# Optimization experiments

Measured on AMD Instinct MI355X. Metric: run time of the kernel, lower is better.

Reference implementation:

```python
import jax, jax.numpy as jnp
import numpy as np

B = 4            # batch size (max batch index + 1, fixed by construction)
H, W = 176, 200  # feature_map_size; x in [0,H), y in [0,W)
C_IN, C_OUT = 128, 256
BW, N = 4096, 64
EPS = 1e-5       # torch LayerNorm default


def setup_inputs() -> dict:
    key = jax.random.key(0)
    k1, k2, k3, k4, k5, k6, k7 = jax.random.split(key, 7)
    window_features = jax.random.normal(k1, (BW, N, C_IN), jnp.float32)
    bidx = jax.random.randint(k2, (BW, N, 1), 0, B)
    xidx = jax.random.randint(k3, (BW, N, 1), -8, H + 8)   # includes invalid coords
    yidx = jax.random.randint(k4, (BW, N, 1), -8, W + 8)
    window_indices = jnp.concatenate([bidx, xidx, yidx], axis=-1).astype(jnp.int32)
    norm_weight = 1.0 + 0.1 * jax.random.normal(k5, (C_IN,), jnp.float32)
    norm_bias = 0.1 * jax.random.normal(k6, (C_IN,), jnp.float32)
    lin_weight = jax.random.normal(k7, (C_OUT, C_IN), jnp.float32) / np.sqrt(C_IN)
    return {"window_features": window_features, "window_indices": window_indices,
            "norm_weight": norm_weight, "norm_bias": norm_bias, "lin_weight": lin_weight}


def reference(window_features, window_indices, norm_weight, norm_bias, lin_weight):
    # window_features: (BW, N, C_IN); window_indices: (BW, N, 3) = (batch, x, y)
    bw, n, c = window_features.shape
    feats = window_features.reshape(-1, c)                # (P, C)
    idx = window_indices.reshape(-1, 3)
    b, x, y = idx[:, 0], idx[:, 1], idx[:, 2]
    valid = (x >= 0) & (x < H) & (y >= 0) & (y < W)

    # unique + index_add_ + sparse-to-dense == scatter-add into dense BEV grid.
    # Invalid rows are routed out-of-bounds and dropped.
    bs = jnp.where(valid, b, B)
    xs = jnp.where(valid, x, 0)
    ys = jnp.where(valid, y, 0)
    # dense layout matches spconv: spatial_shape=[W, H], indices (b, y, x)
    dense_sum = jnp.zeros((B, W, H, c), window_features.dtype)
    dense_sum = dense_sum.at[bs, ys, xs].add(feats, mode="drop")
    count = jnp.zeros((B, W, H), window_features.dtype)
    count = count.at[bs, ys, xs].add(1.0, mode="drop")
    occupied = count > 0                                   # cells holding a unique voxel

    # LayerNorm over C (patch_norm=True) then Linear (bias=False) on occupied cells
    mu = jnp.mean(dense_sum, axis=-1, keepdims=True)
    var = jnp.mean(jnp.square(dense_sum - mu), axis=-1, keepdims=True)
    normed = (dense_sum - mu) * jax.lax.rsqrt(var + EPS) * norm_weight + norm_bias
    dense_out = jnp.einsum("bwhc,oc->bwho", normed, lin_weight)
    dense_out = jnp.where(occupied[..., None], dense_out, 0.0)  # empty cells stay zero

    # gather_operation: pull dense features back to each valid window point
    gathered = dense_out[jnp.where(valid, b, 0), ys, xs]   # (P, C_OUT)
    new_feats = jnp.where(valid[:, None], gathered, 0.0).reshape(bw, n, C_OUT)
    return new_feats, window_indices
```

## Files before the change

kernel.cpp:

```cpp
#include <hip/hip_runtime.h>
#include <stdint.h>

#define HH 176
#define WW 200
#define BB 4
#define CIN 128
#define COUT 256
#define NPTS (4096 * 64)
#define CELLS (BB * WW * HH)
#define FEAT_OUT_ELEMS ((size_t)NPTS * COUT)
#define CAP 32

typedef __attribute__((ext_vector_type(8))) short bf16x8;
typedef __attribute__((ext_vector_type(4))) float f32x4;

__device__ __forceinline__ unsigned short f2bf(float f) {
    union { float f; unsigned int u; } c; c.f = f;
    unsigned int u = c.u;
    u += 0x7fffu + ((u >> 16) & 1u);
    return (unsigned short)(u >> 16);
}
__device__ __forceinline__ float bf2f(unsigned int h16) {
    union { unsigned int u; float f; } c; c.u = h16 << 16;
    return c.f;
}

__global__ __launch_bounds__(256) void build_kernel(
    const int* __restrict__ idx, int* __restrict__ counts, int* __restrict__ plist)
{
    int p = blockIdx.x * 256 + threadIdx.x;
    int b = idx[3 * p], x = idx[3 * p + 1], y = idx[3 * p + 2];
    if ((unsigned)x < HH && (unsigned)y < WW) {
        int cell = (b * WW + y) * HH + x;
        int slot = atomicAdd(&counts[cell], 1);
        if (slot < CAP) plist[(size_t)cell * CAP + slot] = p;
    }
}

__global__ __launch_bounds__(256) void cell_kernel(
    const float* __restrict__ feats, const int* __restrict__ counts,
    const int* __restrict__ plist,
    const float* __restrict__ nw, const float* __restrict__ nb,
    unsigned short* __restrict__ normed)
{
    int cell = blockIdx.x * 4 + (threadIdx.x >> 6);
    int lane = threadIdx.x & 63;
    int n = counts[cell]; n = n < CAP ? n : CAP;
    const int* pl = plist + (size_t)cell * CAP;
    float a0 = 0.0f, a1 = 0.0f;
    for (int i = 0; i < n; ++i) {
        int pid = pl[i];
        float2 v = *(const float2*)(feats + (size_t)pid * CIN + lane * 2);
        a0 += v.x; a1 += v.y;
    }
    float s = a0 + a1;
    float ss = a0 * a0 + a1 * a1;
    #pragma unroll
    for (int m = 32; m >= 1; m >>= 1) {
        s  += __shfl_xor(s, m, 64);
        ss += __shfl_xor(ss, m, 64);
    }
    float mu  = s * (1.0f / 128.0f);
    float var = ss * (1.0f / 128.0f) - mu * mu;
    float inv = rsqrtf(var + 1e-5f);
    float w0 = nw[lane * 2], w1 = nw[lane * 2 + 1];
    float b0 = nb[lane * 2], b1 = nb[lane * 2 + 1];
    ushort2 st;
    st.x = f2bf((a0 - mu) * inv * w0 + b0);
    st.y = f2bf((a1 - mu) * inv * w1 + b1);
    *(ushort2*)(normed + (size_t)cell * CIN + lane * 2) = st;
}

__global__ __launch_bounds__(256) void wcvt_kernel(
    const float* __restrict__ lw, unsigned short* __restrict__ wb)
{
    int i = blockIdx.x * 256 + threadIdx.x;
    wb[i] = f2bf(lw[i]);
}

__global__ __launch_bounds__(256) void gemm_kernel(
    const unsigned short* __restrict__ A,
    const unsigned short* __restrict__ Wb,
    unsigned short* __restrict__ C)
{
    int n0 = blockIdx.x * 64;
    int w = threadIdx.x >> 6;
    int lane = threadIdx.x & 63;
    int l15 = lane & 15;
    int kgrp = (lane >> 4) * 8;

    f32x4 acc[4][4];
    #pragma unroll
    for (int i = 0; i < 4; ++i)
        #pragma unroll
        for (int j = 0; j < 4; ++j)
            acc[i][j] = (f32x4){0.0f, 0.0f, 0.0f, 0.0f};

    const unsigned short* arow[4];
    const unsigned short* brow[4];
    #pragma unroll
    for (int i = 0; i < 4; ++i)
        arow[i] = Wb + (size_t)(((w * 4 + i) * 16 + l15) * CIN) + kgrp;
    #pragma unroll
    for (int j = 0; j < 4; ++j)
        brow[j] = A + (size_t)(n0 + j * 16 + l15) * CIN + kgrp;

    #pragma unroll
    for (int kk = 0; kk < 4; ++kk) {
        bf16x8 a[4], b[4];
        #pragma unroll
        for (int i = 0; i < 4; ++i) a[i] = *(const bf16x8*)(arow[i] + kk * 32);
        #pragma unroll
        for (int j = 0; j < 4; ++j) b[j] = *(const bf16x8*)(brow[j] + kk * 32);
        #pragma unroll
        for (int i = 0; i < 4; ++i)
            #pragma unroll
            for (int j = 0; j < 4; ++j)
                acc[i][j] = __builtin_amdgcn_mfma_f32_16x16x32_bf16(a[i], b[j], acc[i][j], 0, 0, 0);
    }

    int orow = (lane >> 4) * 4;
    #pragma unroll
    for (int j = 0; j < 4; ++j) {
        size_t cell = (size_t)(n0 + j * 16 + l15);
        #pragma unroll
        for (int i = 0; i < 4; ++i) {
            int o = (w * 4 + i) * 16 + orow;
            ushort4 st;
            st.x = f2bf(acc[i][j][0]);
            st.y = f2bf(acc[i][j][1]);
            st.z = f2bf(acc[i][j][2]);
            st.w = f2bf(acc[i][j][3]);
            *(ushort4*)(C + cell * COUT + o) = st;
        }
    }
}

__global__ __launch_bounds__(256) void gather_kernel(
    const unsigned short* __restrict__ Cd, const int* __restrict__ idx,
    float* __restrict__ out_feats, float* __restrict__ out_idx)
{
    int p = blockIdx.x * 4 + (threadIdx.x >> 6);
    int lane = threadIdx.x & 63;
    int b = idx[3 * p], x = idx[3 * p + 1], y = idx[3 * p + 2];
    float4 o = { 0.0f, 0.0f, 0.0f, 0.0f };
    if ((unsigned)x < HH && (unsigned)y < WW) {
        size_t cell = ((size_t)b * WW + y) * HH + x;
        uint2 d = *(const uint2*)(Cd + cell * COUT + lane * 4);
        o.x = bf2f(d.x & 0xffffu);
        o.y = bf2f(d.x >> 16);
        o.z = bf2f(d.y & 0xffffu);
        o.w = bf2f(d.y >> 16);
    }
    *(float4*)(out_feats + (size_t)p * COUT + lane * 4) = o;
    if (lane < 3) out_idx[(size_t)p * 3 + lane] = (float)idx[3 * p + lane];
}

extern "C" void kernel_launch(void* const* d_in, const int* in_sizes, int n_in,
                              void* d_out, int out_size, void* d_ws, size_t ws_size,
                              hipStream_t stream)
{
    const float* feats = (const float*)d_in[0];
    const int*   idx   = (const int*)d_in[1];
    const float* nw    = (const float*)d_in[2];
    const float* nb    = (const float*)d_in[3];
    const float* lw    = (const float*)d_in[4];
    float* out = (float*)d_out;

    char* ws = (char*)d_ws;
    int* counts = (int*)ws;
    int* plist  = (int*)(ws + (1u << 20));
    unsigned short* normed = (unsigned short*)(ws + (20u << 20));
    unsigned short* dout   = (unsigned short*)(ws + (60u << 20));
    unsigned short* wb     = (unsigned short*)(ws + (136u << 20));

    hipMemsetAsync(counts, 0, (size_t)CELLS * 4, stream);
    build_kernel<<<NPTS / 256, 256, 0, stream>>>(idx, counts, plist);
    cell_kernel<<<CELLS / 4, 256, 0, stream>>>(feats, counts, plist, nw, nb, normed);
    wcvt_kernel<<<COUT * CIN / 256, 256, 0, stream>>>(lw, wb);
    gemm_kernel<<<CELLS / 64, 256, 0, stream>>>(normed, wb, dout);
    gather_kernel<<<NPTS / 4, 256, 0, stream>>>(dout, idx, out, out + FEAT_OUT_ELEMS);
}
```

Baseline: 549.2 us.

## Fuse GEMM with direct scatter to points, dropping dense output buffer

The dense per-cell bf16 GEMM output and the separate gather kernel are removed. Each GEMM block now stages its fp32 results in LDS and writes every cell row straight to the output rows of the points in that cell, using the per-cell point lists. A small kernel zeroes the rows of invalid points, and the index copy moves into the build kernel. This is meant to avoid writing and re-reading a large dense intermediate, at the cost of extra block syncs, LDS use and per-cell serial store loops. Points beyond the CAP-sized per-cell list would now be left unwritten.

```diff
diff --git a/kernel.cpp b/kernel.cpp
--- a/kernel.cpp
+++ b/kernel.cpp
@@ -10,6 +10,7 @@
 #define CELLS (BB * WW * HH)
 #define FEAT_OUT_ELEMS ((size_t)NPTS * COUT)
 #define CAP 32
+#define LDSW 260
 
 typedef __attribute__((ext_vector_type(8))) short bf16x8;
 typedef __attribute__((ext_vector_type(4))) float f32x4;
@@ -20,20 +21,32 @@
     u += 0x7fffu + ((u >> 16) & 1u);
     return (unsigned short)(u >> 16);
 }
-__device__ __forceinline__ float bf2f(unsigned int h16) {
-    union { unsigned int u; float f; } c; c.u = h16 << 16;
-    return c.f;
-}
 
 __global__ __launch_bounds__(256) void build_kernel(
-    const int* __restrict__ idx, int* __restrict__ counts, int* __restrict__ plist)
+    const int* __restrict__ idx, int* __restrict__ counts, int* __restrict__ plist,
+    float* __restrict__ out_idx)
 {
     int p = blockIdx.x * 256 + threadIdx.x;
     int b = idx[3 * p], x = idx[3 * p + 1], y = idx[3 * p + 2];
+    out_idx[3 * p]     = (float)b;
+    out_idx[3 * p + 1] = (float)x;
+    out_idx[3 * p + 2] = (float)y;
     if ((unsigned)x < HH && (unsigned)y < WW) {
         int cell = (b * WW + y) * HH + x;
         int slot = atomicAdd(&counts[cell], 1);
         if (slot < CAP) plist[(size_t)cell * CAP + slot] = p;
+    }
+}
+
+__global__ __launch_bounds__(256) void zero_invalid_kernel(
+    const int* __restrict__ idx, float* __restrict__ out_feats)
+{
+    int p = blockIdx.x * 4 + (threadIdx.x >> 6);
+    int lane = threadIdx.x & 63;
+    int x = idx[3 * p + 1], y = idx[3 * p + 2];
+    if (!((unsigned)x < HH && (unsigned)y < WW)) {
+        float4 z = { 0.0f, 0.0f, 0.0f, 0.0f };
+        *(float4*)(out_feats + (size_t)p * COUT + lane * 4) = z;
     }
 }
 
@@ -78,82 +91,89 @@
     wb[i] = f2bf(lw[i]);
 }
 
-__global__ __launch_bounds__(256) void gemm_kernel(
+__global__ __launch_bounds__(256) void gemm_scatter_kernel(
     const unsigned short* __restrict__ A,
     const unsigned short* __restrict__ Wb,
-    unsigned short* __restrict__ C)
-{
+    const int* __restrict__ counts,
+    const int* __restrict__ plist,
+    float* __restrict__ out)
+{
+    __shared__ float lds_out[16 * LDSW];
+    __shared__ int scnt[64];
+    __shared__ int spid[64 * CAP];
+
     int n0 = blockIdx.x * 64;
-    int w = threadIdx.x >> 6;
-    int lane = threadIdx.x & 63;
+    int tid = threadIdx.x;
+    int w = tid >> 6;
+    int lane = tid & 63;
     int l15 = lane & 15;
     int kgrp = (lane >> 4) * 8;
-
-    f32x4 acc[4][4];
+    int orow = (lane >> 4) * 4;
+
+    if (tid < 64) {
+        int cnt = counts[n0 + tid]; cnt = cnt < CAP ? cnt : CAP;
+        scnt[tid] = cnt;
+        for (int s = 0; s < cnt; ++s)
+            spid[tid * CAP + s] = plist[(size_t)(n0 + tid) * CAP + s];
+    }
+
+    bf16x8 a[4][4];
     #pragma unroll
     for (int i = 0; i < 4; ++i)
         #pragma unroll
-        for (int j = 0; j < 4; ++j)
-            acc[i][j] = (f32x4){0.0f, 0.0f, 0.0f, 0.0f};
-
-    const unsigned short* arow[4];
-    const unsigned short* brow[4];
-    #pragma unroll
-    for (int i = 0; i < 4; ++i)
-        arow[i] = Wb + (size_t)(((w * 4 + i) * 16 + l15) * CIN) + kgrp;
-    #pragma unroll
-    for (int j = 0; j < 4; ++j)
-        brow[j] = A + (size_t)(n0 + j * 16 + l15) * CIN + kgrp;
-
-    #pragma unroll
-    for (int kk = 0; kk < 4; ++kk) {
-        bf16x8 a[4], b[4];
-        #pragma unroll
-        for (int i = 0; i < 4; ++i) a[i] = *(const bf16x8*)(arow[i] + kk * 32);
-        #pragma unroll
-        for (int j = 0; j < 4; ++j) b[j] = *(const bf16x8*)(brow[j] + kk * 32);
+        for (int kk = 0; kk < 4; ++kk)
+            a[i][kk] = *(const bf16x8*)(Wb + (size_t)(((w * 4 + i) * 16 + l15) * CIN) + kgrp + kk * 32);
+
+    const unsigned short* bbase = A + (size_t)(n0 + l15) * CIN + kgrp;
+    bf16x8 bcur[4];
+    #pragma unroll
+    for (int kk = 0; kk < 4; ++kk)
+        bcur[kk] = *(const bf16x8*)(bbase + kk * 32);
+
+    __syncthreads();
+
+    #pragma unroll
+    for (int j = 0; j < 4; ++j) {
+        bf16x8 bnext[4];
+        if (j < 3) {
+            #pragma unroll
+            for (int kk = 0; kk < 4; ++kk)
+                bnext[kk] = *(const bf16x8*)(bbase + (size_t)(j + 1) * 16 * CIN + kk * 32);
+        } else {
+            #pragma unroll
+            for (int kk = 0; kk < 4; ++kk) bnext[kk] = bcur[kk];
+        }
+
+        f32x4 acc[4];
+        #pragma unroll
+        for (int i = 0; i < 4; ++i) acc[i] = (f32x4){0.0f, 0.0f, 0.0f, 0.0f};
+        #pragma unroll
+        for (int kk = 0; kk < 4; ++kk)
+            #pragma unroll
+            for (int i = 0; i < 4; ++i)
+                acc[i] = __builtin_amdgcn_mfma_f32_16x16x32_bf16(a[i][kk], bcur[kk], acc[i], 0, 0, 0);
+
         #pragma unroll
         for (int i = 0; i < 4; ++i)
-            #pragma unroll
-            for (int j = 0; j < 4; ++j)
-                acc[i][j] = __builtin_amdgcn_mfma_f32_16x16x32_bf16(a[i], b[j], acc[i][j], 0, 0, 0);
-    }
-
-    int orow = (lane >> 4) * 4;
-    #pragma unroll
-    for (int j = 0; j < 4; ++j) {
-        size_t cell = (size_t)(n0 + j * 16 + l15);
-        #pragma unroll
-        for (int i = 0; i < 4; ++i) {
-            int o = (w * 4 + i) * 16 + orow;
-            ushort4 st;
-            st.x = f2bf(acc[i][j][0]);
-            st.y = f2bf(acc[i][j][1]);
-            st.z = f2bf(acc[i][j][2]);
-            st.w = f2bf(acc[i][j][3]);
-            *(ushort4*)(C + cell * COUT + o) = st;
+            *(f32x4*)(&lds_out[l15 * LDSW + (w * 4 + i) * 16 + orow]) = acc[i];
+
+        __syncthreads();
+
+        int cbase = j * 16;
+        for (int c = 0; c < 16; ++c) {
+            int cnt = scnt[cbase + c];
+            const float* row = &lds_out[c * LDSW];
+            for (int t = 0; t < cnt; ++t) {
+                int pid = spid[(cbase + c) * CAP + t];
+                out[(size_t)pid * COUT + tid] = row[tid];
+            }
         }
-    }
-}
-
-__global__ __launch_bounds__(256) void gather_kernel(
-    const unsigned short* __restrict__ Cd, const int* __restrict__ idx,
-    float* __restrict__ out_feats, float* __restrict__ out_idx)
-{
-    int p = blockIdx.x * 4 + (threadIdx.x >> 6);
-    int lane = threadIdx.x & 63;
-    int b = idx[3 * p], x = idx[3 * p + 1], y = idx[3 * p + 2];
-    float4 o = { 0.0f, 0.0f, 0.0f, 0.0f };
-    if ((unsigned)x < HH && (unsigned)y < WW) {
-        size_t cell = ((size_t)b * WW + y) * HH + x;
-        uint2 d = *(const uint2*)(Cd + cell * COUT + lane * 4);
-        o.x = bf2f(d.x & 0xffffu);
-        o.y = bf2f(d.x >> 16);
-        o.z = bf2f(d.y & 0xffffu);
-        o.w = bf2f(d.y >> 16);
-    }
-    *(float4*)(out_feats + (size_t)p * COUT + lane * 4) = o;
-    if (lane < 3) out_idx[(size_t)p * 3 + lane] = (float)idx[3 * p + lane];
+
+        __syncthreads();
+
+        #pragma unroll
+        for (int kk = 0; kk < 4; ++kk) bcur[kk] = bnext[kk];
+    }
 }
 
 extern "C" void kernel_launch(void* const* d_in, const int* in_sizes, int n_in,
@@ -171,13 +191,12 @@
     int* counts = (int*)ws;
     int* plist  = (int*)(ws + (1u << 20));
     unsigned short* normed = (unsigned short*)(ws + (20u << 20));
-    unsigned short* dout   = (unsigned short*)(ws + (60u << 20));
-    unsigned short* wb     = (unsigned short*)(ws + (136u << 20));
+    unsigned short* wb     = (unsigned short*)(ws + (60u << 20));
 
     hipMemsetAsync(counts, 0, (size_t)CELLS * 4, stream);
-    build_kernel<<<NPTS / 256, 256, 0, stream>>>(idx, counts, plist);
+    zero_invalid_kernel<<<NPTS / 4, 256, 0, stream>>>(idx, out);
+    build_kernel<<<NPTS / 256, 256, 0, stream>>>(idx, counts, plist, out + FEAT_OUT_ELEMS);
     cell_kernel<<<CELLS / 4, 256, 0, stream>>>(feats, counts, plist, nw, nb, normed);
     wcvt_kernel<<<COUT * CIN / 256, 256, 0, stream>>>(lw, wb);
-    gemm_kernel<<<CELLS / 64, 256, 0, stream>>>(normed, wb, dout);
-    gather_kernel<<<NPTS / 4, 256, 0, stream>>>(dout, idx, out, out + FEAT_OUT_ELEMS);
-}
+    gemm_scatter_kernel<<<CELLS / 64, 256, 0, stream>>>(normed, wb, counts, plist, out);
+}
```

Result: faster. 503.5 us (-8.3%).
